# Kernel tuning notes

Measured on AMD Instinct MI355X. Metric: run time of the kernel, lower is better.

The kernel has to match this reference:

```python
import jax, jax.numpy as jnp
import numpy as np

H, DH = 8, 64           # heads, dim_head
SCALE = DH ** -0.5


def setup_inputs() -> dict:
    key = jax.random.key(0)
    ks = jax.random.split(key, 8)
    b, f, n, dim = 16, 8, 256, 512
    inner = H * DH
    w = lambda k, s: jax.random.normal(k, s, jnp.float32) * 0.02
    return {
        "x": jax.random.normal(ks[0], (b, f * n, dim), jnp.float32),
        "external": jax.random.normal(ks[1], (b, 1, dim), jnp.float32),
        "Wq": w(ks[2], (dim, inner)), "bq": jnp.zeros((inner,), jnp.float32),
        "Wk": w(ks[3], (dim, inner)), "bk": jnp.zeros((inner,), jnp.float32),
        "Wv": w(ks[4], (dim, inner)), "bv": jnp.zeros((inner,), jnp.float32),
        "Wo": w(ks[5], (inner, dim)), "bo": jnp.zeros((dim,), jnp.float32),
        "f": f,
    }


def reference(x, external, Wq, bq, Wk, bk, Wv, bv, Wo, bo, f):
    b, N, dim = x.shape          # N = f * n
    n = N // f
    xa = jnp.concatenate([external, x], axis=1)          # (b, N+1, dim)

    def proj(W, bias):
        t = xa @ W + bias                                # (b, N+1, H*DH)
        # 'b n (h d) -> (b h) n d'
        return t.reshape(b, N + 1, H, DH).transpose(0, 2, 1, 3).reshape(b * H, N + 1, DH)

    q = proj(Wq, bq) * SCALE
    k = proj(Wk, bk)
    v = proj(Wv, bv)

    def split_local(t):
        ext = jnp.repeat(t[:, :1], f, axis=0)            # (b*H*f, 1, DH)  'b n d -> (b r) n d'
        loc = t[:, 1:].reshape(b * H * f, n, DH)         # 'b (f n) d -> (b f) n d'
        return jnp.concatenate([ext, loc], axis=1)       # (b*H*f, n+1, DH)

    q_, k_, v_ = split_local(q), split_local(k), split_local(v)

    att = jax.nn.softmax(jnp.einsum('bid,bjd->bij', q_, k_), axis=-1)
    out = jnp.einsum('bij,bjd->bid', att, v_)            # (b*H*f, n+1, DH)

    # external token output: '(b h r) d -> b r (h d)' then take r == 1
    ext_out = out[:, 0].reshape(b, H, f, DH).transpose(0, 2, 1, 3).reshape(b, f, H * DH)
    ext_out = ext_out[:, 1:2]                            # (b, 1, H*DH)

    # local outputs: '(b f) n d -> b (f n) d' then '(b h) n d -> b n (h d)'
    main = out[:, 1:].reshape(b, H, N, DH).transpose(0, 2, 1, 3).reshape(b, N, H * DH)

    return main @ Wo + bo, ext_out @ Wo + bo
```

## Files before the change

### kernel.cpp

```cpp
#include <hip/hip_runtime.h>
#include <stdint.h>

#define ATT_SCALE 0.125f

typedef __attribute__((ext_vector_type(8))) short bhalf8;
typedef __attribute__((ext_vector_type(4))) float floatx4;
typedef __attribute__((ext_vector_type(16))) float floatx16;
typedef __attribute__((ext_vector_type(8))) unsigned short ush8;

__device__ __forceinline__ unsigned short f2bf(float f) {
  union { float f; unsigned int u; } v; v.f = f;
  unsigned int r = v.u + 0x7fffu + ((v.u >> 16) & 1u);
  return (unsigned short)(r >> 16);
}
__device__ __forceinline__ float bf2f(unsigned short u) {
  union { unsigned int u; float f; } v; v.u = ((unsigned int)u) << 16;
  return v.f;
}
__device__ __forceinline__ void glds16(const void* g, void* l) {
  __builtin_amdgcn_global_load_lds(
      (__attribute__((address_space(1))) void*)g,
      (__attribute__((address_space(3))) void*)l, 16, 0, 0);
}

__global__ __launch_bounds__(256) void k_conv_x(const float* __restrict__ x,
                                                unsigned short* __restrict__ out) {
  int i = blockIdx.x * 256 + threadIdx.x;
  float4 v = ((const float4*)x)[i];
  unsigned int lo = (unsigned int)f2bf(v.x) | ((unsigned int)f2bf(v.y) << 16);
  unsigned int hi = (unsigned int)f2bf(v.z) | ((unsigned int)f2bf(v.w) << 16);
  ((uint2*)out)[i] = make_uint2(lo, hi);
}

__global__ __launch_bounds__(256) void k_conv_w(
    const float* __restrict__ Wq, const float* __restrict__ Wk,
    const float* __restrict__ Wv, const float* __restrict__ Wo,
    const float* __restrict__ bq, const float* __restrict__ bk, const float* __restrict__ bv,
    unsigned short* __restrict__ Wqkvt, unsigned short* __restrict__ Wot,
    float* __restrict__ biasqkv) {
  int idx = blockIdx.x * 256 + threadIdx.x;
  {
    int nn = idx >> 9, k = idx & 511;
    const float* W = (nn < 512) ? Wq : ((nn < 1024) ? Wk : Wv);
    int n = nn & 511;
    Wqkvt[idx] = f2bf(W[k * 512 + n]);
  }
  if (idx < 512 * 512) {
    int n = idx >> 9, k = idx & 511;
    Wot[idx] = f2bf(Wo[k * 512 + n]);
  }
  if (idx < 1536) {
    biasqkv[idx] = (idx < 512) ? bq[idx] : ((idx < 1024) ? bk[idx - 512] : bv[idx - 1024]);
  }
}

__global__ __launch_bounds__(256) void k_ext_qkv(
    const float* __restrict__ ext,
    const float* __restrict__ Wq, const float* __restrict__ Wk, const float* __restrict__ Wv,
    const float* __restrict__ bq, const float* __restrict__ bk, const float* __restrict__ bv,
    float* __restrict__ EQKV) {
  int b = blockIdx.x / 6, c = blockIdx.x % 6;
  int nn = c * 256 + threadIdx.x;
  __shared__ float xs[512];
  xs[threadIdx.x] = ext[b * 512 + threadIdx.x];
  xs[256 + threadIdx.x] = ext[b * 512 + 256 + threadIdx.x];
  __syncthreads();
  const float* W; const float* bias; float scale = 1.f; int n;
  if (nn < 512)      { W = Wq; bias = bq; n = nn;        scale = ATT_SCALE; }
  else if (nn < 1024){ W = Wk; bias = bk; n = nn - 512; }
  else               { W = Wv; bias = bv; n = nn - 1024; }
  float acc = 0.f;
  #pragma unroll 8
  for (int k = 0; k < 512; ++k) acc += xs[k] * W[k * 512 + n];
  EQKV[b * 1536 + nn] = (acc + bias[n]) * scale;
}

template <int EPI>
__global__ __launch_bounds__(256, 2) void k_gemm(
    const unsigned short* __restrict__ A, const unsigned short* __restrict__ B,
    const float* __restrict__ bias, void* __restrict__ Cptr, int N, int nbn) {
  __shared__ __align__(16) unsigned short S[16384];
  int tid = threadIdx.x, lane = tid & 63, wv = tid >> 6;
  int lo = lane & 15, hi = lane >> 4;
  int waveM = wv >> 1, waveN = wv & 1;

  int nwg = gridDim.x;
  int wg = (blockIdx.x & 7) * (nwg >> 3) + (blockIdx.x >> 3);
  int bm = wg / nbn, bn = wg % nbn;

  const unsigned short* Ab = A + (size_t)bm * 128 * 512;
  const unsigned short* Bb = B + (size_t)bn * 128 * 512;
  unsigned short* lA = S;
  unsigned short* lB = S + 8192;

  floatx4 acc[4][4];
  #pragma unroll
  for (int m = 0; m < 4; ++m)
    #pragma unroll
    for (int n = 0; n < 4; ++n) acc[m][n] = floatx4{0.f, 0.f, 0.f, 0.f};

  for (int kt = 0; kt < 8; ++kt) {
    __syncthreads();
    #pragma unroll
    for (int i = 0; i < 4; ++i) {
      int chunk = i * 256 + tid;
      int row = chunk >> 3, slot = chunk & 7;
      glds16(Ab + (size_t)row * 512 + kt * 64 + ((slot ^ (row & 7)) << 3),
             lA + (size_t)(i * 256 + wv * 64) * 8);
    }
    #pragma unroll
    for (int i = 0; i < 4; ++i) {
      int chunk = i * 256 + tid;
      int row = chunk >> 3, slot = chunk & 7;
      glds16(Bb + (size_t)row * 512 + kt * 64 + ((slot ^ (row & 7)) << 3),
             lB + (size_t)(i * 256 + wv * 64) * 8);
    }
    __syncthreads();

    bhalf8 af[4][2], bf4[4][2];
    #pragma unroll
    for (int m = 0; m < 4; ++m) {
      int row = waveM * 64 + m * 16 + lo;
      #pragma unroll
      for (int ks = 0; ks < 2; ++ks)
        af[m][ks] = *(const bhalf8*)(lA + (size_t)row * 64 + (((ks * 4 + hi) ^ (row & 7)) << 3));
    }
    #pragma unroll
    for (int n = 0; n < 4; ++n) {
      int row = waveN * 64 + n * 16 + lo;
      #pragma unroll
      for (int ks = 0; ks < 2; ++ks)
        bf4[n][ks] = *(const bhalf8*)(lB + (size_t)row * 64 + (((ks * 4 + hi) ^ (row & 7)) << 3));
    }
    #pragma unroll
    for (int m = 0; m < 4; ++m)
      #pragma unroll
      for (int n = 0; n < 4; ++n) {
        acc[m][n] = __builtin_amdgcn_mfma_f32_16x16x32_bf16(af[m][0], bf4[n][0], acc[m][n], 0, 0, 0);
        acc[m][n] = __builtin_amdgcn_mfma_f32_16x16x32_bf16(af[m][1], bf4[n][1], acc[m][n], 0, 0, 0);
      }
  }

  #pragma unroll
  for (int m = 0; m < 4; ++m) {
    int row0 = bm * 128 + waveM * 64 + m * 16 + hi * 4;
    #pragma unroll
    for (int n = 0; n < 4; ++n) {
      int col = bn * 128 + waveN * 64 + n * 16 + lo;
      float bb = bias[col];
      #pragma unroll
      for (int r = 0; r < 4; ++r) {
        float v = acc[m][n][r] + bb;
        if constexpr (EPI == 0) {
          if (col < 512) v *= ATT_SCALE;
          ((unsigned short*)Cptr)[(size_t)(row0 + r) * N + col] = f2bf(v);
        } else {
          ((float*)Cptr)[(size_t)(row0 + r) * N + col] = v;
        }
      }
    }
  }
}

#define VTC 296
__global__ __launch_bounds__(512, 4) void k_attn(
    const unsigned short* __restrict__ QKV,
    const float* __restrict__ EQKV,
    unsigned short* __restrict__ mainb) {
  __shared__ __align__(16) unsigned short Ks[288 * 64];
  __shared__ __align__(16) unsigned short Vt[64 * VTC];
  int g = blockIdx.x;
  int b = g >> 6, h = (g >> 3) & 7, j = g & 7;
  int tid = threadIdx.x, lane = tid & 63, wv = tid >> 6;
  int ql = lane & 31, hb = lane >> 5;
  const size_t rowbase = (size_t)b * 2048 + (size_t)j * 256;
  const unsigned short* Kg = QKV + rowbase * 1536 + 512 + h * 64;
  const unsigned short* Vg = QKV + rowbase * 1536 + 1024 + h * 64;

  int qbase = wv * 32;
  const unsigned short* qp = QKV + (rowbase + qbase + ql) * 1536 + h * 64 + hb * 8;
  bhalf8 qf[4];
  #pragma unroll
  for (int c = 0; c < 4; ++c) qf[c] = *(const bhalf8*)(qp + c * 16);

  {
    ush8 z8 = {0, 0, 0, 0, 0, 0, 0, 0};
    for (int c = tid; c < (64 * VTC) / 8; c += 512) ((ush8*)Vt)[c] = z8;
  }
  __syncthreads();

  {
    int keybase = 1 + wv * 32;
    #pragma unroll
    for (int i = 0; i < 4; ++i) {
      int key = keybase + i * 8 + (lane >> 3);
      int slot = lane & 7;
      const unsigned short* src =
          Kg + (size_t)(key - 1) * 1536 + (((slot * 16) ^ ((key & 7) << 4)) >> 1);
      glds16(src, &Ks[(size_t)(keybase + i * 8) * 64]);
    }
  }
  for (int c = tid; c < 2048; c += 512) {
    int key = 1 + (c & 255), d0 = (c >> 8) * 8;
    ush8 vv = *(const ush8*)(Vg + (size_t)(key - 1) * 1536 + d0);
    #pragma unroll
    for (int u = 0; u < 8; ++u) Vt[(d0 + u) * VTC + key] = vv[u];
  }
  if (wv == 0) {
    Ks[lane] = f2bf(EQKV[b * 1536 + 512 + h * 64 + lane]);
    Vt[lane * VTC] = f2bf(EQKV[b * 1536 + 1024 + h * 64 + lane]);
  }
  __syncthreads();

  floatx16 o0, o1;
  #pragma unroll
  for (int i = 0; i < 16; ++i) { o0[i] = 0.f; o1[i] = 0.f; }
  float m = -1e30f, lsum = 0.f;

  #pragma unroll
  for (int t = 0; t < 9; ++t) {
    floatx16 s;
    #pragma unroll
    for (int i = 0; i < 16; ++i) s[i] = 0.f;
    int key = t * 32 + ql;
    #pragma unroll
    for (int c = 0; c < 4; ++c) {
      bhalf8 kf = *(const bhalf8*)((const char*)Ks + key * 128 +
                                   ((c * 32 + hb * 16) ^ ((key & 7) << 4)));
      s = __builtin_amdgcn_mfma_f32_32x32x16_bf16(kf, qf[c], s, 0, 0, 0);
    }
    if (t == 8) {
      #pragma unroll
      for (int r = 0; r < 16; ++r) {
        if (r == 0) { if (hb != 0) s[0] = -1e30f; }
        else s[r] = -1e30f;
      }
    }
    float mt = s[0];
    #pragma unroll
    for (int r = 1; r < 16; ++r) mt = fmaxf(mt, s[r]);
    mt = fmaxf(mt, __shfl_xor(mt, 32, 64));
    if (!__all(mt - m <= 8.f)) {
      float mnew = fmaxf(m, mt);
      float corr = __expf(m - mnew);
      lsum *= corr;
      #pragma unroll
      for (int r = 0; r < 16; ++r) { o0[r] *= corr; o1[r] *= corr; }
      m = mnew;
    }
    float p[16]; float ts = 0.f;
    #pragma unroll
    for (int r = 0; r < 16; ++r) { p[r] = __expf(s[r] - m); ts += p[r]; }
    lsum += ts;
    unsigned int pk[8], qk[8];
    #pragma unroll
    for (int i = 0; i < 8; ++i)
      pk[i] = (unsigned int)f2bf(p[2 * i]) | ((unsigned int)f2bf(p[2 * i + 1]) << 16);
    #pragma unroll
    for (int i = 0; i < 8; ++i) qk[i] = __shfl_xor(pk[i], 32, 64);
    bhalf8 f0, f1;
    unsigned int* f0u = (unsigned int*)&f0;
    unsigned int* f1u = (unsigned int*)&f1;
    if (hb == 0) {
      f0u[0] = pk[0]; f0u[1] = pk[1]; f0u[2] = qk[0]; f0u[3] = qk[1];
      f1u[0] = pk[4]; f1u[1] = pk[5]; f1u[2] = qk[4]; f1u[3] = qk[5];
    } else {
      f0u[0] = qk[2]; f0u[1] = qk[3]; f0u[2] = pk[2]; f0u[3] = pk[3];
      f1u[0] = qk[6]; f1u[1] = qk[7]; f1u[2] = pk[6]; f1u[3] = pk[7];
    }
    {
      const char* vb0 = (const char*)Vt + ((0 * 32 + ql) * VTC + t * 32 + hb * 8) * 2;
      bhalf8 v0 = *(const bhalf8*)vb0;
      bhalf8 v1 = *(const bhalf8*)(vb0 + 32);
      o0 = __builtin_amdgcn_mfma_f32_32x32x16_bf16(v0, f0, o0, 0, 0, 0);
      o0 = __builtin_amdgcn_mfma_f32_32x32x16_bf16(v1, f1, o0, 0, 0, 0);
      const char* vb1 = (const char*)Vt + ((1 * 32 + ql) * VTC + t * 32 + hb * 8) * 2;
      bhalf8 w0 = *(const bhalf8*)vb1;
      bhalf8 w1 = *(const bhalf8*)(vb1 + 32);
      o1 = __builtin_amdgcn_mfma_f32_32x32x16_bf16(w0, f0, o1, 0, 0, 0);
      o1 = __builtin_amdgcn_mfma_f32_32x32x16_bf16(w1, f1, o1, 0, 0, 0);
    }
  }

  lsum += __shfl_xor(lsum, 32, 64);
  float rinv = 1.f / lsum;
  __syncthreads();
  char* ob = (char*)(Ks + wv * 2048);
  #pragma unroll
  for (int dt = 0; dt < 2; ++dt) {
    #pragma unroll
    for (int i = 0; i < 8; ++i) {
      int d0 = dt * 32 + ((2 * i) & 3) + 8 * (i >> 1) + 4 * hb;
      float a = (dt ? o1[2 * i] : o0[2 * i]) * rinv;
      float c = (dt ? o1[2 * i + 1] : o0[2 * i + 1]) * rinv;
      unsigned int w = (unsigned int)f2bf(a) | ((unsigned int)f2bf(c) << 16);
      *(unsigned int*)(ob + ql * 128 + ((d0 * 2) ^ ((ql & 7) << 4))) = w;
    }
  }
  #pragma unroll
  for (int i = 0; i < 4; ++i) {
    int chunk = i * 64 + lane;
    int q = chunk >> 3, slot = chunk & 7;
    bhalf8 vv = *(const bhalf8*)(ob + q * 128 + ((slot * 16) ^ ((q & 7) << 4)));
    *(bhalf8*)(mainb + (rowbase + qbase + q) * 512 + h * 64 + slot * 8) = vv;
  }
}

__global__ __launch_bounds__(256) void k_ext_attn(
    const unsigned short* __restrict__ QKV, const float* __restrict__ EQKV,
    float* __restrict__ extpre) {
  int b = blockIdx.x >> 3, h = blockIdx.x & 7;
  int tid = threadIdx.x, lane = tid & 63, wv = tid >> 6;
  __shared__ float qs[64];
  __shared__ float ps[257];
  __shared__ float red[8];
  __shared__ float acc4[4][64];
  if (tid < 64) qs[tid] = EQKV[b * 1536 + h * 64 + tid];
  __syncthreads();
  const size_t base = (size_t)b * 2048 + 256;
  float sc[2] = {-1e30f, -1e30f};
  #pragma unroll
  for (int it = 0; it < 2; ++it) {
    int key = tid + it * 256;
    if (key < 257) {
      float s = 0.f;
      if (key == 0) {
        const float* kr = EQKV + b * 1536 + 512 + h * 64;
        #pragma unroll 8
        for (int d = 0; d < 64; ++d) s += qs[d] * kr[d];
      } else {
        const unsigned short* kr = QKV + (base + key - 1) * 1536 + 512 + h * 64;
        #pragma unroll
        for (int c = 0; c < 8; ++c) {
          ush8 kv = *(const ush8*)(kr + c * 8);
          #pragma unroll
          for (int u = 0; u < 8; ++u) s += qs[c * 8 + u] * bf2f(kv[u]);
        }
      }
      sc[it] = s;
    }
  }
  float lmax = fmaxf(sc[0], sc[1]);
  for (int d = 1; d < 64; d <<= 1) lmax = fmaxf(lmax, __shfl_xor(lmax, d, 64));
  if (lane == 0) red[wv] = lmax;
  __syncthreads();
  float M = fmaxf(fmaxf(red[0], red[1]), fmaxf(red[2], red[3]));
  float lsum = 0.f;
  #pragma unroll
  for (int it = 0; it < 2; ++it) {
    int key = tid + it * 256;
    if (key < 257) { float p = __expf(sc[it] - M); ps[key] = p; lsum += p; }
  }
  for (int d = 1; d < 64; d <<= 1) lsum += __shfl_xor(lsum, d, 64);
  if (lane == 0) red[4 + wv] = lsum;
  __syncthreads();
  float S = red[4] + red[5] + red[6] + red[7];
  int d = tid & 63, part = tid >> 6;
  float acc = 0.f;
  for (int key = part; key < 257; key += 4) {
    float vv = (key == 0) ? EQKV[b * 1536 + 1024 + h * 64 + d]
                          : bf2f(QKV[(base + key - 1) * 1536 + 1024 + h * 64 + d]);
    acc += ps[key] * vv;
  }
  acc4[part][d] = acc;
  __syncthreads();
  if (tid < 64) {
    float r = (acc4[0][tid] + acc4[1][tid] + acc4[2][tid] + acc4[3][tid]) / S;
    extpre[b * 512 + h * 64 + tid] = r;
  }
}

__global__ __launch_bounds__(256) void k_ext_out(
    const float* __restrict__ extpre, const float* __restrict__ Wo,
    const float* __restrict__ bo, float* __restrict__ out) {
  int b = blockIdx.x, half = blockIdx.y;
  int n = half * 256 + threadIdx.x;
  __shared__ float xs[512];
  xs[threadIdx.x] = extpre[b * 512 + threadIdx.x];
  xs[256 + threadIdx.x] = extpre[b * 512 + 256 + threadIdx.x];
  __syncthreads();
  float acc = bo[n];
  #pragma unroll 8
  for (int k = 0; k < 512; ++k) acc += xs[k] * Wo[k * 512 + n];
  out[16777216 + b * 512 + n] = acc;
}

extern "C" void kernel_launch(void* const* d_in, const int* in_sizes, int n_in,
                              void* d_out, int out_size, void* d_ws, size_t ws_size,
                              hipStream_t stream) {
  (void)in_sizes; (void)n_in; (void)out_size; (void)ws_size;
  const float* x   = (const float*)d_in[0];
  const float* ext = (const float*)d_in[1];
  const float* Wq  = (const float*)d_in[2];
  const float* bq  = (const float*)d_in[3];
  const float* Wk  = (const float*)d_in[4];
  const float* bk  = (const float*)d_in[5];
  const float* Wv  = (const float*)d_in[6];
  const float* bv  = (const float*)d_in[7];
  const float* Wo  = (const float*)d_in[8];
  const float* bo  = (const float*)d_in[9];
  float* out = (float*)d_out;

  char* ws = (char*)d_ws;
  size_t off = 0;
  auto take = [&](size_t bytes) { char* p = ws + off; off += (bytes + 255) & ~(size_t)255; return p; };
  unsigned short* Xbf    = (unsigned short*)take((size_t)32768 * 512 * 2);
  unsigned short* Wqkvt  = (unsigned short*)take((size_t)1536 * 512 * 2);
  unsigned short* Wot    = (unsigned short*)take((size_t)512 * 512 * 2);
  float*          biasqkv= (float*)take(1536 * 4);
  float*          EQKV   = (float*)take(16 * 1536 * 4);
  unsigned short* QKVb   = (unsigned short*)take((size_t)32768 * 1536 * 2);
  unsigned short* mainb  = (unsigned short*)take((size_t)32768 * 512 * 2);
  float*          extpre = (float*)take(16 * 512 * 4);

  k_conv_x<<<16384, 256, 0, stream>>>(x, Xbf);
  k_conv_w<<<3072, 256, 0, stream>>>(Wq, Wk, Wv, Wo, bq, bk, bv, Wqkvt, Wot, biasqkv);
  k_ext_qkv<<<96, 256, 0, stream>>>(ext, Wq, Wk, Wv, bq, bk, bv, EQKV);
  k_gemm<0><<<3072, 256, 0, stream>>>(Xbf, Wqkvt, biasqkv, QKVb, 1536, 12);
  k_attn<<<1024, 512, 0, stream>>>(QKVb, EQKV, mainb);
  k_ext_attn<<<128, 256, 0, stream>>>(QKVb, EQKV, extpre);
  k_gemm<1><<<1024, 256, 0, stream>>>(mainb, Wot, bo, out, 512, 4);
  k_ext_out<<<dim3(16, 2), 256, 0, stream>>>(extpre, Wo, bo, out);
}
```

Baseline: 222.0 us.

## Fuse fp32-to-bf16 conversion of x into QKV GEMM and double-buffer LDS in GEMMs

Removes the separate x conversion kernel. The QKV GEMM now loads fp32 x directly into registers, converts it with packed bf16 conversion instructions, and writes it into swizzled LDS. Both GEMMs now use double-buffered LDS, issuing the next K-tile's loads before the current MFMA work so memory overlaps compute. This cuts a full read and write of the bf16 copy of x. The cost is twice the LDS per block (64KB), which may limit occupancy, and the QKV GEMM now reads twice as many bytes of A per tile.

```diff
diff --git a/kernel.cpp b/kernel.cpp
--- a/kernel.cpp
+++ b/kernel.cpp
@@ -17,19 +17,15 @@
   union { unsigned int u; float f; } v; v.u = ((unsigned int)u) << 16;
   return v.f;
 }
+__device__ __forceinline__ unsigned int pk2(float a, float b) {
+  unsigned int r;
+  asm("v_cvt_pk_bf16_f32 %0, %1, %2" : "=v"(r) : "v"(a), "v"(b));
+  return r;
+}
 __device__ __forceinline__ void glds16(const void* g, void* l) {
   __builtin_amdgcn_global_load_lds(
       (__attribute__((address_space(1))) void*)g,
       (__attribute__((address_space(3))) void*)l, 16, 0, 0);
-}
-
-__global__ __launch_bounds__(256) void k_conv_x(const float* __restrict__ x,
-                                                unsigned short* __restrict__ out) {
-  int i = blockIdx.x * 256 + threadIdx.x;
-  float4 v = ((const float4*)x)[i];
-  unsigned int lo = (unsigned int)f2bf(v.x) | ((unsigned int)f2bf(v.y) << 16);
-  unsigned int hi = (unsigned int)f2bf(v.z) | ((unsigned int)f2bf(v.w) << 16);
-  ((uint2*)out)[i] = make_uint2(lo, hi);
 }
 
 __global__ __launch_bounds__(256) void k_conv_w(
@@ -75,47 +71,68 @@
   EQKV[b * 1536 + nn] = (acc + bias[n]) * scale;
 }
 
-template <int EPI>
-__global__ __launch_bounds__(256, 2) void k_gemm(
-    const unsigned short* __restrict__ A, const unsigned short* __restrict__ B,
-    const float* __restrict__ bias, void* __restrict__ Cptr, int N, int nbn) {
-  __shared__ __align__(16) unsigned short S[16384];
+__global__ __launch_bounds__(256, 2) void k_gemm_qkv(
+    const float* __restrict__ X, const unsigned short* __restrict__ B,
+    const float* __restrict__ bias, unsigned short* __restrict__ C) {
+  __shared__ __align__(16) unsigned short S[32768];
   int tid = threadIdx.x, lane = tid & 63, wv = tid >> 6;
   int lo = lane & 15, hi = lane >> 4;
   int waveM = wv >> 1, waveN = wv & 1;
 
   int nwg = gridDim.x;
   int wg = (blockIdx.x & 7) * (nwg >> 3) + (blockIdx.x >> 3);
-  int bm = wg / nbn, bn = wg % nbn;
-
-  const unsigned short* Ab = A + (size_t)bm * 128 * 512;
+  int bm = wg / 12, bn = wg % 12;
+
+  const float* Xb = X + (size_t)bm * 128 * 512;
   const unsigned short* Bb = B + (size_t)bn * 128 * 512;
-  unsigned short* lA = S;
-  unsigned short* lB = S + 8192;
-
-  floatx4 acc[4][4];
-  #pragma unroll
-  for (int m = 0; m < 4; ++m)
-    #pragma unroll
-    for (int n = 0; n < 4; ++n) acc[m][n] = floatx4{0.f, 0.f, 0.f, 0.f};
-
-  for (int kt = 0; kt < 8; ++kt) {
-    __syncthreads();
+  int arow = tid >> 1, ahalf = tid & 1;
+  const float* xrow = Xb + (size_t)arow * 512 + ahalf * 32;
+
+  float4 fA[8];
+  auto loadA = [&](int kt) {
+    #pragma unroll
+    for (int i = 0; i < 8; ++i) fA[i] = *(const float4*)(xrow + kt * 64 + i * 4);
+  };
+  auto stageB = [&](int kt, int c) {
+    unsigned short* lB = S + 16384 + c * 8192;
     #pragma unroll
     for (int i = 0; i < 4; ++i) {
-      int chunk = i * 256 + tid;
-      int row = chunk >> 3, slot = chunk & 7;
-      glds16(Ab + (size_t)row * 512 + kt * 64 + ((slot ^ (row & 7)) << 3),
-             lA + (size_t)(i * 256 + wv * 64) * 8);
-    }
-    #pragma unroll
-    for (int i = 0; i < 4; ++i) {
-      int chunk = i * 256 + tid;
-      int row = chunk >> 3, slot = chunk & 7;
+      int chunk = i * 256 + tid, row = chunk >> 3, slot = chunk & 7;
       glds16(Bb + (size_t)row * 512 + kt * 64 + ((slot ^ (row & 7)) << 3),
              lB + (size_t)(i * 256 + wv * 64) * 8);
     }
-    __syncthreads();
+  };
+  auto writeA = [&](int c) {
+    unsigned short* lA = S + c * 8192;
+    #pragma unroll
+    for (int j = 0; j < 4; ++j) {
+      uint4 w;
+      w.x = pk2(fA[2 * j].x, fA[2 * j].y);
+      w.y = pk2(fA[2 * j].z, fA[2 * j].w);
+      w.z = pk2(fA[2 * j + 1].x, fA[2 * j + 1].y);
+      w.w = pk2(fA[2 * j + 1].z, fA[2 * j + 1].w);
+      *(uint4*)((char*)lA + arow * 128 + (((ahalf * 4 + j) ^ (arow & 7)) << 4)) = w;
+    }
+  };
+
+  floatx4 acc[4][4];
+  #pragma unroll
+  for (int m = 0; m < 4; ++m)
+    #pragma unroll
+    for (int n = 0; n < 4; ++n) acc[m][n] = floatx4{0.f, 0.f, 0.f, 0.f};
+
+  loadA(0);
+  stageB(0, 0);
+  asm volatile("s_waitcnt vmcnt(0)" ::: "memory");
+  writeA(0);
+  asm volatile("s_waitcnt lgkmcnt(0)" ::: "memory");
+  __builtin_amdgcn_sched_barrier(0);
+  __builtin_amdgcn_s_barrier();
+
+  for (int t = 0; t < 8; ++t) {
+    const unsigned short* lA = S + (t & 1) * 8192;
+    const unsigned short* lB = S + 16384 + (t & 1) * 8192;
+    if (t < 7) { loadA(t + 1); stageB(t + 1, (t + 1) & 1); }
 
     bhalf8 af[4][2], bf4[4][2];
     #pragma unroll
@@ -139,6 +156,15 @@
         acc[m][n] = __builtin_amdgcn_mfma_f32_16x16x32_bf16(af[m][0], bf4[n][0], acc[m][n], 0, 0, 0);
         acc[m][n] = __builtin_amdgcn_mfma_f32_16x16x32_bf16(af[m][1], bf4[n][1], acc[m][n], 0, 0, 0);
       }
+
+    if (t < 7) {
+      __builtin_amdgcn_sched_barrier(0);
+      asm volatile("s_waitcnt vmcnt(0)" ::: "memory");
+      writeA((t + 1) & 1);
+      asm volatile("s_waitcnt lgkmcnt(0)" ::: "memory");
+      __builtin_amdgcn_sched_barrier(0);
+      __builtin_amdgcn_s_barrier();
+    }
   }
 
   #pragma unroll
@@ -151,13 +177,101 @@
       #pragma unroll
       for (int r = 0; r < 4; ++r) {
         float v = acc[m][n][r] + bb;
-        if constexpr (EPI == 0) {
-          if (col < 512) v *= ATT_SCALE;
-          ((unsigned short*)Cptr)[(size_t)(row0 + r) * N + col] = f2bf(v);
-        } else {
-          ((float*)Cptr)[(size_t)(row0 + r) * N + col] = v;
-        }
+        if (col < 512) v *= ATT_SCALE;
+        C[(size_t)(row0 + r) * 1536 + col] = f2bf(v);
       }
+    }
+  }
+}
+
+__global__ __launch_bounds__(256, 2) void k_gemm_out(
+    const unsigned short* __restrict__ A, const unsigned short* __restrict__ B,
+    const float* __restrict__ bias, float* __restrict__ C) {
+  __shared__ __align__(16) unsigned short S[32768];
+  int tid = threadIdx.x, lane = tid & 63, wv = tid >> 6;
+  int lo = lane & 15, hi = lane >> 4;
+  int waveM = wv >> 1, waveN = wv & 1;
+
+  int nwg = gridDim.x;
+  int wg = (blockIdx.x & 7) * (nwg >> 3) + (blockIdx.x >> 3);
+  int bm = wg / 4, bn = wg % 4;
+
+  const unsigned short* Ab = A + (size_t)bm * 128 * 512;
+  const unsigned short* Bb = B + (size_t)bn * 128 * 512;
+
+  auto stage = [&](int kt, int c) {
+    unsigned short* lA = S + c * 8192;
+    unsigned short* lB = S + 16384 + c * 8192;
+    #pragma unroll
+    for (int i = 0; i < 4; ++i) {
+      int chunk = i * 256 + tid, row = chunk >> 3, slot = chunk & 7;
+      glds16(Ab + (size_t)row * 512 + kt * 64 + ((slot ^ (row & 7)) << 3),
+             lA + (size_t)(i * 256 + wv * 64) * 8);
+    }
+    #pragma unroll
+    for (int i = 0; i < 4; ++i) {
+      int chunk = i * 256 + tid, row = chunk >> 3, slot = chunk & 7;
+      glds16(Bb + (size_t)row * 512 + kt * 64 + ((slot ^ (row & 7)) << 3),
+             lB + (size_t)(i * 256 + wv * 64) * 8);
+    }
+  };
+
+  floatx4 acc[4][4];
+  #pragma unroll
+  for (int m = 0; m < 4; ++m)
+    #pragma unroll
+    for (int n = 0; n < 4; ++n) acc[m][n] = floatx4{0.f, 0.f, 0.f, 0.f};
+
+  stage(0, 0);
+  asm volatile("s_waitcnt vmcnt(0)" ::: "memory");
+  __builtin_amdgcn_s_barrier();
+
+  for (int t = 0; t < 8; ++t) {
+    const unsigned short* lA = S + (t & 1) * 8192;
+    const unsigned short* lB = S + 16384 + (t & 1) * 8192;
+    if (t < 7) stage(t + 1, (t + 1) & 1);
+
+    bhalf8 af[4][2], bf4[4][2];
+    #pragma unroll
+    for (int m = 0; m < 4; ++m) {
+      int row = waveM * 64 + m * 16 + lo;
+      #pragma unroll
+      for (int ks = 0; ks < 2; ++ks)
+        af[m][ks] = *(const bhalf8*)(lA + (size_t)row * 64 + (((ks * 4 + hi) ^ (row & 7)) << 3));
+    }
+    #pragma unroll
+    for (int n = 0; n < 4; ++n) {
+      int row = waveN * 64 + n * 16 + lo;
+      #pragma unroll
+      for (int ks = 0; ks < 2; ++ks)
+        bf4[n][ks] = *(const bhalf8*)(lB + (size_t)row * 64 + (((ks * 4 + hi) ^ (row & 7)) << 3));
+    }
+    #pragma unroll
+    for (int m = 0; m < 4; ++m)
+      #pragma unroll
+      for (int n = 0; n < 4; ++n) {
+        acc[m][n] = __builtin_amdgcn_mfma_f32_16x16x32_bf16(af[m][0], bf4[n][0], acc[m][n], 0, 0, 0);
+        acc[m][n] = __builtin_amdgcn_mfma_f32_16x16x32_bf16(af[m][1], bf4[n][1], acc[m][n], 0, 0, 0);
+      }
+
+    if (t < 7) {
+      __builtin_amdgcn_sched_barrier(0);
+      asm volatile("s_waitcnt vmcnt(0)" ::: "memory");
+      __builtin_amdgcn_sched_barrier(0);
+      __builtin_amdgcn_s_barrier();
+    }
+  }
+
+  #pragma unroll
+  for (int m = 0; m < 4; ++m) {
+    int row0 = bm * 128 + waveM * 64 + m * 16 + hi * 4;
+    #pragma unroll
+    for (int n = 0; n < 4; ++n) {
+      int col = bn * 128 + waveN * 64 + n * 16 + lo;
+      float bb = bias[col];
+      #pragma unroll
+      for (int r = 0; r < 4; ++r)
+        C[(size_t)(row0 + r) * 512 + col] = acc[m][n][r] + bb;
     }
   }
 }
@@ -404,7 +518,6 @@
   char* ws = (char*)d_ws;
   size_t off = 0;
   auto take = [&](size_t bytes) { char* p = ws + off; off += (bytes + 255) & ~(size_t)255; return p; };
-  unsigned short* Xbf    = (unsigned short*)take((size_t)32768 * 512 * 2);
   unsigned short* Wqkvt  = (unsigned short*)take((size_t)1536 * 512 * 2);
   unsigned short* Wot    = (unsigned short*)take((size_t)512 * 512 * 2);
   float*          biasqkv= (float*)take(1536 * 4);
@@ -413,12 +526,11 @@
   unsigned short* mainb  = (unsigned short*)take((size_t)32768 * 512 * 2);
   float*          extpre = (float*)take(16 * 512 * 4);
 
-  k_conv_x<<<16384, 256, 0, stream>>>(x, Xbf);
   k_conv_w<<<3072, 256, 0, stream>>>(Wq, Wk, Wv, Wo, bq, bk, bv, Wqkvt, Wot, biasqkv);
   k_ext_qkv<<<96, 256, 0, stream>>>(ext, Wq, Wk, Wv, bq, bk, bv, EQKV);
-  k_gemm<0><<<3072, 256, 0, stream>>>(Xbf, Wqkvt, biasqkv, QKVb, 1536, 12);
+  k_gemm_qkv<<<3072, 256, 0, stream>>>(x, Wqkvt, biasqkv, QKVb);
   k_attn<<<1024, 512, 0, stream>>>(QKVb, EQKV, mainb);
   k_ext_attn<<<128, 256, 0, stream>>>(QKVb, EQKV, extpre);
-  k_gemm<1><<<1024, 256, 0, stream>>>(mainb, Wot, bo, out, 512, 4);
+  k_gemm_out<<<1024, 256, 0, stream>>>(mainb, Wot, bo, out);
   k_ext_out<<<dim3(16, 2), 256, 0, stream>>>(extpre, Wo, bo, out);
 }
```

Result: slower. 280.5 us (+26.4%).
